# Kernel optimization log

Measured on AMD Instinct MI355X. Metric: run time of the kernel, lower is better.

## Reference

```python
import jax, jax.numpy as jnp
import numpy as np

NUM_BUCKETS = 320
MAX_DISTANCE = 800


def _layer_norm(x, w, b, eps=1e-5):
    x32 = x.astype(jnp.float32)
    mu = x32.mean(-1, keepdims=True)
    var = x32.var(-1, keepdims=True)
    return ((x32 - mu) / jnp.sqrt(var + eps) * w + b).astype(x.dtype)


def _rel_pos_bucket(rel):
    half = NUM_BUCKETS // 2            # 160
    st = half // 2                     # 80 (small threshold)
    sign = (rel >= 0).astype(jnp.int32)
    ab = jnp.abs(rel)
    is_small = ab < st
    log_ratio = jnp.log(jnp.clip(ab.astype(jnp.float32), 1.0) / st) / np.float32(np.log(MAX_DISTANCE / st))
    log_pos = st + (log_ratio * (half - st)).astype(jnp.int32)  # trunc toward zero like .long()
    log_pos = jnp.minimum(log_pos, half - 1)
    bucket = jnp.where(is_small, ab, log_pos) + sign * half
    return jnp.clip(bucket, 0, NUM_BUCKETS - 1)


def setup_inputs() -> dict:
    key = jax.random.key(0)
    B, T, C, H, FF = 2, 2048, 768, 12, 3072
    D = C // H
    ks = jax.random.split(key, 16)
    s = 0.02
    return {
        "x": jax.random.normal(ks[0], (B, T, C), jnp.float32),
        "ln1_w": jnp.ones((C,), jnp.float32),
        "ln1_b": jnp.zeros((C,), jnp.float32),
        "wq": jax.random.normal(ks[1], (C, C), jnp.float32) * s,
        "bq": jnp.zeros((C,), jnp.float32),
        "wk": jax.random.normal(ks[2], (C, C), jnp.float32) * s,
        "bk": jnp.zeros((C,), jnp.float32),
        "wv": jax.random.normal(ks[3], (C, C), jnp.float32) * s,
        "bv": jnp.zeros((C,), jnp.float32),
        "wo": jax.random.normal(ks[4], (C, C), jnp.float32) * s,
        "bo": jnp.zeros((C,), jnp.float32),
        "ln2_w": jnp.ones((C,), jnp.float32),
        "ln2_b": jnp.zeros((C,), jnp.float32),
        "w1": jax.random.normal(ks[5], (FF, C), jnp.float32) * s,
        "b1": jnp.zeros((FF,), jnp.float32),
        "w2": jax.random.normal(ks[6], (C, FF), jnp.float32) * s,
        "b2": jnp.zeros((C,), jnp.float32),
        "rel_embed": jax.random.normal(ks[7], (NUM_BUCKETS, H), jnp.float32),
        "gate_ur_w": jax.random.normal(ks[8], (H, D), jnp.float32) * 0.01,
        "gate_i_w": jax.random.normal(ks[9], (H, D), jnp.float32) * 0.01,
        "rel_scale": jnp.ones((H,), jnp.float32),
    }


def reference(x, ln1_w, ln1_b, wq, bq, wk, bk, wv, bv, wo, bo,
              ln2_w, ln2_b, w1, b1, w2, b2, rel_embed, gate_ur_w, gate_i_w, rel_scale):
    B, T, C = x.shape
    H = rel_embed.shape[1]
    D = C // H

    residual = x
    h = _layer_norm(x, ln1_w, ln1_b)
    q = (h @ wq.T + bq).reshape(B, T, H, D).transpose(0, 2, 1, 3)  # [B,H,T,D]
    k = (h @ wk.T + bk).reshape(B, T, H, D).transpose(0, 2, 1, 3)
    v = (h @ wv.T + bv).reshape(B, T, H, D).transpose(0, 2, 1, 3)

    attn = jnp.einsum('bhqd,bhkd->bhqk', q, k) * (D ** -0.5)

    # gated relative position bias
    pos = jnp.arange(T)
    rel = pos[None, :] - pos[:, None]                 # [T,T]
    buckets = _rel_pos_bucket(rel)                    # [T,T]
    pe = rel_embed[buckets]                           # [T,T,H]
    pe = jnp.transpose(pe, (2, 0, 1))[None]           # [1,H,T,T]
    g_in = q.mean(axis=2).transpose(0, 2, 1).mean(axis=-1)   # [B,D]
    gate_r = jax.nn.sigmoid(g_in @ gate_ur_w.T)       # [B,H]
    gate_u = jax.nn.sigmoid(g_in @ gate_i_w.T)        # [B,H]
    gate = 1.0 + (gate_u * rel_scale[None, :] * gate_r)[:, :, None, None]
    bias = pe * gate                                  # [B,H,T,T]

    attn = jax.nn.softmax(attn + bias, axis=-1)
    out = jnp.einsum('bhqk,bhkd->bhqd', attn, v).transpose(0, 2, 1, 3).reshape(B, T, C)
    x = residual + out @ wo.T + bo

    residual = x
    h = _layer_norm(x, ln2_w, ln2_b)
    h = jax.nn.gelu(h @ w1.T + b1, approximate=False) @ w2.T + b2
    return residual + h
```

## Files before the change

### kernel.cpp

```cpp
#include <hip/hip_runtime.h>
#include <hip/hip_bf16.h>


#define Tn 2048
#define Cn 768
#define Hn 12
#define Dn 64
#define FFn 3072
#define Mn 4096
#define QKVS 2304
#define LQK 1536

typedef __attribute__((ext_vector_type(8))) short bfrag;
typedef __attribute__((ext_vector_type(8))) unsigned short us8;
typedef __attribute__((ext_vector_type(4))) float f32x4;

#define GLDS(gptr, lptr) __builtin_amdgcn_global_load_lds( \
    (const __attribute__((address_space(1))) void*)(gptr), \
    (__attribute__((address_space(3))) void*)(lptr), 16, 0, 0)

__device__ __forceinline__ unsigned short f2bu(float f){
  __hip_bfloat16 h = __float2bfloat16(f);
  return *(unsigned short*)&h;
}
__device__ __forceinline__ float bu2f(unsigned short u){
  union { unsigned int i; float f; } v; v.i = ((unsigned int)u) << 16; return v.f;
}
__device__ __forceinline__ us8 pack8(float4 a, float4 b){
  us8 c;
  c[0]=f2bu(a.x); c[1]=f2bu(a.y); c[2]=f2bu(a.z); c[3]=f2bu(a.w);
  c[4]=f2bu(b.x); c[5]=f2bu(b.y); c[6]=f2bu(b.z); c[7]=f2bu(b.w);
  return c;
}
__device__ __forceinline__ float fexp2(float x){ return __builtin_amdgcn_exp2f(x); }

__device__ __forceinline__ float block_reduce_sum(float v, float* sred){
  #pragma unroll
  for (int off = 32; off > 0; off >>= 1) v += __shfl_down(v, off, 64);
  __syncthreads();
  if ((threadIdx.x & 63) == 0) sred[threadIdx.x >> 6] = v;
  __syncthreads();
  return sred[0] + sred[1] + sred[2] + sred[3];
}

__global__ __launch_bounds__(256) void cast_all_kernel(
    const float* __restrict__ wq, const float* __restrict__ wk,
    const float* __restrict__ wv, const float* __restrict__ wo,
    const float* __restrict__ w1, const float* __restrict__ w2,
    const float* __restrict__ bq, const float* __restrict__ bk,
    const float* __restrict__ bv,
    unsigned short* __restrict__ Wqkv, unsigned short* __restrict__ Wob,
    unsigned short* __restrict__ W1b, unsigned short* __restrict__ W2b,
    float* __restrict__ bqkv)
{
  const int blk = blockIdx.x;
  if (blk >= 3456){
    const int i = (blk - 3456) * 256 + threadIdx.x;
    bqkv[i] = (i < Cn) ? bq[i] : (i < 2 * Cn) ? bk[i - Cn] : bv[i - 2 * Cn];
    return;
  }
  const float* src; unsigned short* dst; int i;
  if (blk < 288)      { src = wq; dst = Wqkv;               i = blk * 256 + threadIdx.x; }
  else if (blk < 576) { src = wk; dst = Wqkv + Cn * Cn;     i = (blk - 288) * 256 + threadIdx.x; }
  else if (blk < 864) { src = wv; dst = Wqkv + 2 * Cn * Cn; i = (blk - 576) * 256 + threadIdx.x; }
  else if (blk < 1152){ src = wo; dst = Wob;                i = (blk - 864) * 256 + threadIdx.x; }
  else if (blk < 2304){ src = w1; dst = W1b;                i = (blk - 1152) * 256 + threadIdx.x; }
  else                { src = w2; dst = W2b;                i = (blk - 2304) * 256 + threadIdx.x; }
  const float4 a = ((const float4*)src)[i * 2];
  const float4 b = ((const float4*)src)[i * 2 + 1];
  *(us8*)&dst[i * 8] = pack8(a, b);
}

__global__ __launch_bounds__(256) void ln_kernel(const float* __restrict__ xin,
    const float* __restrict__ w, const float* __restrict__ bsh,
    unsigned short* __restrict__ out)
{
  __shared__ float xs[Cn];
  __shared__ float sred[4];
  const size_t base = (size_t)blockIdx.x * Cn;
  float s = 0.f;
  for (int c = threadIdx.x; c < Cn; c += 256){
    float v = xin[base + c];
    xs[c] = v; s += v;
  }
  const float mean = block_reduce_sum(s, sred) * (1.f / Cn);
  float s2 = 0.f;
  for (int c = threadIdx.x; c < Cn; c += 256){
    float d = xs[c] - mean; s2 += d * d;
  }
  const float var = block_reduce_sum(s2, sred) * (1.f / Cn);
  const float rstd = rsqrtf(var + 1e-5f);
  for (int c = threadIdx.x; c < Cn; c += 256)
    out[base + c] = f2bu((xs[c] - mean) * rstd * w[c] + bsh[c]);
}

template<int EPI, bool TRANSV>
__global__ __launch_bounds__(256) void gemm_mfma_kernel(
    const unsigned short* __restrict__ A, const unsigned short* __restrict__ Bw,
    const float* __restrict__ bias, unsigned short* __restrict__ vt,
    void* __restrict__ Cout, int M, int N, int K, int ldo)
{
  __shared__ __align__(16) unsigned short As[128 * 32];
  __shared__ __align__(16) unsigned short Bs[128 * 32];
  const int tid = threadIdx.x;
  const int lane = tid & 63, w = tid >> 6;
  const int nl = lane & 15, quad = lane >> 4;
  const int wm = w >> 1, wn = w & 1;
  const int bm = blockIdx.y * 128, bn = blockIdx.x * 128;
  const int l4 = lane >> 2, lk = (lane & 3) * 8;

  f32x4 acc[4][4];
  #pragma unroll
  for (int i = 0; i < 4; i++)
    #pragma unroll
    for (int j = 0; j < 4; j++) acc[i][j] = (f32x4){0.f, 0.f, 0.f, 0.f};

  const int c0 = w, c1 = w + 4;
  const unsigned short* A0 = A + (size_t)(bm + c0 * 16 + l4) * K + lk;
  const unsigned short* A1 = A + (size_t)(bm + c1 * 16 + l4) * K + lk;
  const unsigned short* B0 = Bw + (size_t)(bn + c0 * 16 + l4) * K + lk;
  const unsigned short* B1 = Bw + (size_t)(bn + c1 * 16 + l4) * K + lk;

  for (int k0 = 0; k0 < K; k0 += 32){
    __syncthreads();
    GLDS(A0 + k0, &As[c0 * 512]); GLDS(A1 + k0, &As[c1 * 512]);
    GLDS(B0 + k0, &Bs[c0 * 512]); GLDS(B1 + k0, &Bs[c1 * 512]);
    __syncthreads();
    bfrag Af[4], Bf[4];
    #pragma unroll
    for (int mt = 0; mt < 4; mt++)
      Af[mt] = *(const bfrag*)&As[(wm * 64 + mt * 16 + nl) * 32 + quad * 8];
    #pragma unroll
    for (int nt = 0; nt < 4; nt++)
      Bf[nt] = *(const bfrag*)&Bs[(wn * 64 + nt * 16 + nl) * 32 + quad * 8];
    #pragma unroll
    for (int mt = 0; mt < 4; mt++)
      #pragma unroll
      for (int nt = 0; nt < 4; nt++)
        acc[mt][nt] = __builtin_amdgcn_mfma_f32_16x16x32_bf16(Af[mt], Bf[nt], acc[mt][nt], 0, 0, 0);
  }

  if (TRANSV && bn >= 1536){
    #pragma unroll
    for (int nt = 0; nt < 4; nt++){
      const int col = bn + wn * 64 + nt * 16 + nl;
      const float bv_ = bias[col];
      const int vcol = col - 1536;
      #pragma unroll
      for (int mt = 0; mt < 4; mt++){
        const int row0 = bm + wm * 64 + mt * 16 + quad * 4;
        unsigned short pk[4];
        #pragma unroll
        for (int r = 0; r < 4; r++) pk[r] = f2bu(acc[mt][nt][r] + bv_);
        *(uint2*)&vt[(size_t)vcol * Mn + row0] = *(uint2*)pk;
      }
    }
    return;
  }
  #pragma unroll
  for (int nt = 0; nt < 4; nt++){
    const int col = bn + wn * 64 + nt * 16 + nl;
    const float bv_ = bias[col];
    #pragma unroll
    for (int mt = 0; mt < 4; mt++){
      const int row0 = bm + wm * 64 + mt * 16 + quad * 4;
      #pragma unroll
      for (int r = 0; r < 4; r++){
        const size_t idx = (size_t)(row0 + r) * ldo + col;
        const float v = acc[mt][nt][r] + bv_;
        if (EPI == 2){
          ((unsigned short*)Cout)[idx] = f2bu(0.5f * v * (1.f + erff(v * 0.70710678118f)));
        } else {
          ((unsigned short*)Cout)[idx] = f2bu(v);
        }
      }
    }
  }
}

__global__ __launch_bounds__(256) void gemm_t64_kernel(
    const unsigned short* __restrict__ A, const unsigned short* __restrict__ Bw,
    const float* __restrict__ bias, const float* __restrict__ res,
    float* __restrict__ Cout, int M, int N, int K)
{
  __shared__ __align__(16) unsigned short As[64 * 32];
  __shared__ __align__(16) unsigned short Bs[64 * 32];
  const int tid = threadIdx.x;
  const int lane = tid & 63, w = tid >> 6;
  const int nl = lane & 15, quad = lane >> 4;
  const int bm = blockIdx.y * 64, bn = blockIdx.x * 64;
  const int l4 = lane >> 2, lk = (lane & 3) * 8;

  f32x4 acc[4];
  #pragma unroll
  for (int j = 0; j < 4; j++) acc[j] = (f32x4){0.f, 0.f, 0.f, 0.f};

  const unsigned short* A0 = A + (size_t)(bm + w * 16 + l4) * K + lk;
  const unsigned short* B0 = Bw + (size_t)(bn + w * 16 + l4) * K + lk;

  for (int k0 = 0; k0 < K; k0 += 32){
    __syncthreads();
    GLDS(A0 + k0, &As[w * 512]);
    GLDS(B0 + k0, &Bs[w * 512]);
    __syncthreads();
    const bfrag Af = *(const bfrag*)&As[(w * 16 + nl) * 32 + quad * 8];
    bfrag Bf[4];
    #pragma unroll
    for (int nt = 0; nt < 4; nt++)
      Bf[nt] = *(const bfrag*)&Bs[(nt * 16 + nl) * 32 + quad * 8];
    #pragma unroll
    for (int nt = 0; nt < 4; nt++)
      acc[nt] = __builtin_amdgcn_mfma_f32_16x16x32_bf16(Af, Bf[nt], acc[nt], 0, 0, 0);
  }

  const int row0 = bm + w * 16 + quad * 4;
  #pragma unroll
  for (int nt = 0; nt < 4; nt++){
    const int col = bn + nt * 16 + nl;
    const float bv_ = bias[col];
    #pragma unroll
    for (int r = 0; r < 4; r++){
      const size_t idx = (size_t)(row0 + r) * N + col;
      Cout[idx] = acc[nt][r] + bv_ + res[idx];
    }
  }
}

__global__ __launch_bounds__(256) void qmean_part_kernel(
    const unsigned short* __restrict__ QKVqk, float* __restrict__ qpart)
{
  __shared__ float ps[Cn];
  const int b = blockIdx.y, t0 = blockIdx.x * 128;
  const int tid = threadIdx.x;
  float a0 = 0.f, a1 = 0.f, a2 = 0.f;
  for (int r = 0; r < 128; r++){
    const size_t base = (size_t)(b * Tn + t0 + r) * LQK;
    a0 += bu2f(QKVqk[base + tid]);
    a1 += bu2f(QKVqk[base + tid + 256]);
    a2 += bu2f(QKVqk[base + tid + 512]);
  }
  ps[tid] = a0; ps[tid + 256] = a1; ps[tid + 512] = a2;
  __syncthreads();
  if (tid < Dn){
    float s = 0.f;
    #pragma unroll
    for (int hh = 0; hh < Hn; hh++) s += ps[hh * Dn + tid];
    qpart[(b * 16 + blockIdx.x) * Dn + tid] = s;
  }
}

__global__ __launch_bounds__(64) void gate_kernel(const float* __restrict__ qpart,
    const float* __restrict__ gur, const float* __restrict__ gi,
    const float* __restrict__ rsc, float* __restrict__ gate)
{
  const int b = blockIdx.x / Hn, h = blockIdx.x % Hn;
  const int d = threadIdx.x;
  float s = 0.f;
  #pragma unroll
  for (int blk = 0; blk < 16; blk++) s += qpart[(b * 16 + blk) * Dn + d];
  const float g = s * (1.f / (Hn * Tn));
  float vr = g * gur[h * Dn + d];
  float vu = g * gi[h * Dn + d];
  #pragma unroll
  for (int off = 32; off > 0; off >>= 1){
    vr += __shfl_down(vr, off, 64);
    vu += __shfl_down(vu, off, 64);
  }
  if (d == 0){
    const float gr = 1.f / (1.f + __expf(-vr));
    const float gu = 1.f / (1.f + __expf(-vu));
    gate[blockIdx.x] = 1.f + gu * rsc[h] * gr;
  }
}

__global__ void bias_kernel(const float* __restrict__ rel_embed,
                            float* __restrict__ bias_rel)
{
  const int idx = blockIdx.x * 256 + threadIdx.x;
  if (idx >= 4095) return;
  const int rel = idx - 2047;
  const int ab = rel < 0 ? -rel : rel;
  int bucket;
  if (ab < 80){
    bucket = ab;
  } else {
    const float lr = logf((float)ab * (1.0f / 80.0f)) * (1.0f / 2.3025851f);
    int lp = 80 + (int)(lr * 80.0f);
    bucket = lp < 159 ? lp : 159;
  }
  if (rel >= 0) bucket += 160;
  #pragma unroll
  for (int h = 0; h < Hn; h++)
    bias_rel[h * 4095 + idx] = rel_embed[bucket * Hn + h] * 1.44269504089f;
}

__global__ __launch_bounds__(256) void attn_mfma_kernel(
    const unsigned short* __restrict__ QKVqk, const unsigned short* __restrict__ VT,
    const float* __restrict__ bias_rel, const float* __restrict__ gate,
    unsigned short* __restrict__ O)
{
  __shared__ __align__(16) char smem[9216 * 4 + 1024];
  unsigned short* Qs = (unsigned short*)smem;
  float* bias_blk    = (float*)smem;
  unsigned short* Ks = (unsigned short*)(smem + 9216);
  unsigned short* Vt = (unsigned short*)(smem + 18432);
  unsigned short* Ptq = (unsigned short*)(smem + 27648);
  float* lsh         = (float*)(smem + 36864);

  const int qbase = blockIdx.x * 64;
  const int h = blockIdx.y, b = blockIdx.z;
  const int tid = threadIdx.x;
  const float g = gate[b * Hn + h];
  const float* brow = bias_rel + h * 4095 + 1984 - qbase;
  const unsigned short* Q = QKVqk;
  const unsigned short* K = QKVqk + Cn;

  {
    const int row = tid >> 2, cg = (tid & 3) * 16;
    const us8* qp = (const us8*)(Q + (size_t)(b * Tn + qbase + row) * LQK + h * Dn + cg);
    *(us8*)&Qs[row * 72 + cg]     = qp[0];
    *(us8*)&Qs[row * 72 + cg + 8] = qp[1];
  }
  __syncthreads();

  const int lane = tid & 63, w = tid >> 6;
  const int nl = lane & 15, quad = lane >> 4;

  bfrag Qb[4][2];
  #pragma unroll
  for (int mt = 0; mt < 4; mt++){
    Qb[mt][0] = *(const bfrag*)&Qs[(mt * 16 + nl) * 72 + quad * 8];
    Qb[mt][1] = *(const bfrag*)&Qs[(mt * 16 + nl) * 72 + 32 + quad * 8];
  }
  __syncthreads();
  for (int j = tid; j < 2111; j += 256) bias_blk[j] = brow[j] * g;

  const int wq = w & 1, wd = w >> 1;
  f32x4 Oa[2][2];
  #pragma unroll
  for (int a = 0; a < 2; a++)
    #pragma unroll
    for (int d0 = 0; d0 < 2; d0++) Oa[a][d0] = (f32x4){0.f, 0.f, 0.f, 0.f};
  float l_part[4] = {0.f, 0.f, 0.f, 0.f};

  const int skey = tid >> 2, sdg = (tid & 3) * 16;
  const int vd = tid >> 3, vk8 = (tid & 7) * 8;
  const unsigned short* vtg = VT + (size_t)(h * Dn) * Mn + (size_t)b * Tn;

  for (int kt = 0; kt < 32; kt++){
    const int kbase = kt * 64;
    __syncthreads();
    {
      const us8* kp = (const us8*)(K + (size_t)(b * Tn + kbase + skey) * LQK + h * Dn + sdg);
      *(us8*)&Ks[skey * 72 + sdg]     = kp[0];
      *(us8*)&Ks[skey * 72 + sdg + 8] = kp[1];
    }
    {
      const us8 v0 = *(const us8*)&vtg[(size_t)vd * Mn + kbase + vk8];
      const us8 v1 = *(const us8*)&vtg[(size_t)(32 + vd) * Mn + kbase + vk8];
      *(us8*)&Vt[vd * 72 + vk8]        = v0;
      *(us8*)&Vt[(32 + vd) * 72 + vk8] = v1;
    }
    __syncthreads();

    const bfrag Ka0 = *(const bfrag*)&Ks[(w * 16 + nl) * 72 + quad * 8];
    const bfrag Ka1 = *(const bfrag*)&Ks[(w * 16 + nl) * 72 + 32 + quad * 8];
    const int bofs = kbase + w * 16 + quad * 4 + 63 - nl;
    #pragma unroll
    for (int mt = 0; mt < 4; mt++){
      f32x4 z = (f32x4){0.f, 0.f, 0.f, 0.f};
      z = __builtin_amdgcn_mfma_f32_16x16x32_bf16(Ka0, Qb[mt][0], z, 0, 0, 0);
      z = __builtin_amdgcn_mfma_f32_16x16x32_bf16(Ka1, Qb[mt][1], z, 0, 0, 0);
      unsigned short pk[4];
      #pragma unroll
      for (int r = 0; r < 4; r++){
        const float p = fexp2(z[r] * 0.18033688f + bias_blk[bofs - mt * 16 + r]);
        l_part[mt] += p;
        pk[r] = f2bu(p);
      }
      *(uint2*)&Ptq[(mt * 16 + nl) * 72 + w * 16 + quad * 4] = *(uint2*)pk;
    }
    __syncthreads();

    bfrag Vf[2][2], Pf[2][2];
    #pragma unroll
    for (int d0 = 0; d0 < 2; d0++){
      const int dt = wd * 2 + d0;
      Vf[d0][0] = *(const bfrag*)&Vt[(dt * 16 + nl) * 72 + quad * 8];
      Vf[d0][1] = *(const bfrag*)&Vt[(dt * 16 + nl) * 72 + 32 + quad * 8];
    }
    #pragma unroll
    for (int a = 0; a < 2; a++){
      const int qt = wq * 2 + a;
      Pf[a][0] = *(const bfrag*)&Ptq[(qt * 16 + nl) * 72 + quad * 8];
      Pf[a][1] = *(const bfrag*)&Ptq[(qt * 16 + nl) * 72 + 32 + quad * 8];
    }
    #pragma unroll
    for (int a = 0; a < 2; a++)
      #pragma unroll
      for (int d0 = 0; d0 < 2; d0++){
        Oa[a][d0] = __builtin_amdgcn_mfma_f32_16x16x32_bf16(Vf[d0][0], Pf[a][0], Oa[a][d0], 0, 0, 0);
        Oa[a][d0] = __builtin_amdgcn_mfma_f32_16x16x32_bf16(Vf[d0][1], Pf[a][1], Oa[a][d0], 0, 0, 0);
      }
  }

  #pragma unroll
  for (int mt = 0; mt < 4; mt++){
    float l = l_part[mt];
    l += __shfl_xor(l, 16, 64);
    l += __shfl_xor(l, 32, 64);
    if (quad == 0) lsh[w * 64 + mt * 16 + nl] = l;
  }
  __syncthreads();
  #pragma unroll
  for (int a = 0; a < 2; a++){
    const int q = (wq * 2 + a) * 16 + nl;
    const float linv = 1.f / (lsh[q] + lsh[64 + q] + lsh[128 + q] + lsh[192 + q]);
    unsigned short* orow = O + (size_t)(b * Tn + qbase + q) * Cn + h * Dn;
    #pragma unroll
    for (int d0 = 0; d0 < 2; d0++){
      unsigned short pk[4];
      #pragma unroll
      for (int r = 0; r < 4; r++) pk[r] = f2bu(Oa[a][d0][r] * linv);
      *(uint2*)&orow[(wd * 2 + d0) * 16 + quad * 4] = *(uint2*)pk;
    }
  }
}

extern "C" void kernel_launch(void* const* d_in, const int* in_sizes, int n_in,
                              void* d_out, int out_size, void* d_ws, size_t ws_size,
                              hipStream_t stream)
{
  const float* x     = (const float*)d_in[0];
  const float* ln1_w = (const float*)d_in[1];
  const float* ln1_b = (const float*)d_in[2];
  const float* wq    = (const float*)d_in[3];
  const float* bq    = (const float*)d_in[4];
  const float* wk    = (const float*)d_in[5];
  const float* bk    = (const float*)d_in[6];
  const float* wv    = (const float*)d_in[7];
  const float* bv    = (const float*)d_in[8];
  const float* wo    = (const float*)d_in[9];
  const float* bo    = (const float*)d_in[10];
  const float* ln2_w = (const float*)d_in[11];
  const float* ln2_b = (const float*)d_in[12];
  const float* w1    = (const float*)d_in[13];
  const float* b1    = (const float*)d_in[14];
  const float* w2    = (const float*)d_in[15];
  const float* b2    = (const float*)d_in[16];
  const float* rel_embed = (const float*)d_in[17];
  const float* gur   = (const float*)d_in[18];
  const float* gi    = (const float*)d_in[19];
  const float* rsc   = (const float*)d_in[20];

  char* ws = (char*)d_ws;
  unsigned short* QKVqk = (unsigned short*)(ws);
  unsigned short* VT    = (unsigned short*)(ws + 12582912);
  unsigned short* Ob    = (unsigned short*)(ws + 18874368);
  float*          X2    = (float*)(ws + 25165824);
  unsigned short* Hb    = (unsigned short*)(ws + 37748736);
  unsigned short* Wqkv  = (unsigned short*)(ws + 44040192);
  unsigned short* Wob   = (unsigned short*)(ws + 47579136);
  unsigned short* W1b   = (unsigned short*)(ws + 48758784);
  unsigned short* W2b   = (unsigned short*)(ws + 53477376);
  float*          bqkv  = (float*)(ws + 58195968);
  float*          bias_rel = (float*)(ws + 58205184);
  float*          qpart = (float*)(ws + 58401744);
  float*          gate  = (float*)(ws + 58409936);
  unsigned short* Fb    = (unsigned short*)(ws);

  cast_all_kernel<<<3465, 256, 0, stream>>>(wq, wk, wv, wo, w1, w2, bq, bk, bv,
                                            Wqkv, Wob, W1b, W2b, bqkv);
  ln_kernel<<<Mn, 256, 0, stream>>>(x, ln1_w, ln1_b, Hb);
  gemm_mfma_kernel<0, true><<<dim3(QKVS / 128, Mn / 128), 256, 0, stream>>>(
      Hb, Wqkv, bqkv, VT, QKVqk, Mn, QKVS, Cn, LQK);
  qmean_part_kernel<<<dim3(16, 2), 256, 0, stream>>>(QKVqk, qpart);
  gate_kernel<<<2 * Hn, 64, 0, stream>>>(qpart, gur, gi, rsc, gate);
  bias_kernel<<<16, 256, 0, stream>>>(rel_embed, bias_rel);
  attn_mfma_kernel<<<dim3(Tn / 64, Hn, 2), 256, 0, stream>>>(QKVqk, VT, bias_rel, gate, Ob);
  gemm_t64_kernel<<<dim3(Cn / 64, Mn / 64), 256, 0, stream>>>(
      Ob, Wob, bo, x, X2, Mn, Cn, Cn);
  ln_kernel<<<Mn, 256, 0, stream>>>(X2, ln2_w, ln2_b, Hb);
  gemm_mfma_kernel<2, false><<<dim3(FFn / 128, Mn / 128), 256, 0, stream>>>(
      Hb, W1b, b1, nullptr, Fb, Mn, FFn, Cn, FFn);
  gemm_t64_kernel<<<dim3(Cn / 64, Mn / 64), 256, 0, stream>>>(
      Fb, W2b, b2, X2, (float*)d_out, Mn, Cn, FFn);
}
```

Baseline: 356.3 us.

## Precompute fragment-ordered rel-pos bias table and swizzle GEMM block order

Replaces the per-head 1D bias vector, which each attention block staged into LDS, with a larger table precomputed inside the cast kernel. The table is laid out per (head, q-block diagonal, k-offset, lane) so each lane reads a float4 directly from global memory. This removes the LDS staging, its sync and the scalar LDS reads, and drops the separate bias kernel launch. The gate multiply becomes an fma, and the GEMM kernels now remap a 1D grid so consecutive blocks share B tiles for better L2 reuse. The cost is a ~5MB bias table read from global/L2 inside the attention inner loop.

```diff
diff --git a/kernel.cpp b/kernel.cpp
--- a/kernel.cpp
+++ b/kernel.cpp
@@ -43,20 +43,52 @@
   return sred[0] + sred[1] + sred[2] + sred[3];
 }
 
+__device__ __forceinline__ int rel_bucket(int rel){
+  const int ab = rel < 0 ? -rel : rel;
+  int bucket;
+  if (ab < 80){
+    bucket = ab;
+  } else {
+    const float lr = logf((float)ab * (1.0f / 80.0f)) * (1.0f / 2.3025851f);
+    int lp = 80 + (int)(lr * 80.0f);
+    bucket = lp < 159 ? lp : 159;
+  }
+  if (rel >= 0) bucket += 160;
+  return bucket;
+}
+
 __global__ __launch_bounds__(256) void cast_all_kernel(
     const float* __restrict__ wq, const float* __restrict__ wk,
     const float* __restrict__ wv, const float* __restrict__ wo,
     const float* __restrict__ w1, const float* __restrict__ w2,
     const float* __restrict__ bq, const float* __restrict__ bk,
-    const float* __restrict__ bv,
+    const float* __restrict__ bv, const float* __restrict__ rel_embed,
     unsigned short* __restrict__ Wqkv, unsigned short* __restrict__ Wob,
     unsigned short* __restrict__ W1b, unsigned short* __restrict__ W2b,
-    float* __restrict__ bqkv)
+    float* __restrict__ biasT, float* __restrict__ bqkv)
 {
   const int blk = blockIdx.x;
+  if (blk >= 3787){
+    const int i = (blk - 3787) * 256 + threadIdx.x;
+    bqkv[i] = (i < Cn) ? bq[i] : (i < 2 * Cn) ? bk[i - Cn] : bv[i - 2 * Cn];
+    return;
+  }
   if (blk >= 3456){
-    const int i = (blk - 3456) * 256 + threadIdx.x;
-    bqkv[i] = (i < Cn) ? bq[i] : (i < 2 * Cn) ? bk[i - Cn] : bv[i - 2 * Cn];
+    const int f4 = (blk - 3456) * 256 + threadIdx.x;
+    if (f4 >= 84672) return;
+    int t = f4;
+    const int nl = t & 15; t >>= 4;
+    const int quad = t & 3; t >>= 2;
+    const int dmi = t % 7; t /= 7;
+    const int di = t % 63; t /= 63;
+    const int h = t;
+    const int rbase = 64 * (di - 31) + 16 * (dmi - 3) + quad * 4 - nl;
+    float4 o;
+    o.x = rel_embed[rel_bucket(rbase + 0) * Hn + h] * 1.44269504089f;
+    o.y = rel_embed[rel_bucket(rbase + 1) * Hn + h] * 1.44269504089f;
+    o.z = rel_embed[rel_bucket(rbase + 2) * Hn + h] * 1.44269504089f;
+    o.w = rel_embed[rel_bucket(rbase + 3) * Hn + h] * 1.44269504089f;
+    ((float4*)biasT)[f4] = o;
     return;
   }
   const float* src; unsigned short* dst; int i;
@@ -106,7 +138,9 @@
   const int lane = tid & 63, w = tid >> 6;
   const int nl = lane & 15, quad = lane >> 4;
   const int wm = w >> 1, wn = w & 1;
-  const int bm = blockIdx.y * 128, bn = blockIdx.x * 128;
+  const int id = blockIdx.x;
+  const int bm = ((id & 7) * 4 + ((id >> 3) & 3)) * 128;
+  const int bn = (id >> 5) * 128;
   const int l4 = lane >> 2, lk = (lane & 3) * 8;
 
   f32x4 acc[4][4];
@@ -188,7 +222,9 @@
   const int tid = threadIdx.x;
   const int lane = tid & 63, w = tid >> 6;
   const int nl = lane & 15, quad = lane >> 4;
-  const int bm = blockIdx.y * 64, bn = blockIdx.x * 64;
+  const int id = blockIdx.x;
+  const int bm = ((id & 7) * 8 + ((id >> 3) & 7)) * 64;
+  const int bn = (id >> 6) * 64;
   const int l4 = lane >> 2, lk = (lane & 3) * 8;
 
   f32x4 acc[4];
@@ -273,45 +309,21 @@
   }
 }
 
-__global__ void bias_kernel(const float* __restrict__ rel_embed,
-                            float* __restrict__ bias_rel)
-{
-  const int idx = blockIdx.x * 256 + threadIdx.x;
-  if (idx >= 4095) return;
-  const int rel = idx - 2047;
-  const int ab = rel < 0 ? -rel : rel;
-  int bucket;
-  if (ab < 80){
-    bucket = ab;
-  } else {
-    const float lr = logf((float)ab * (1.0f / 80.0f)) * (1.0f / 2.3025851f);
-    int lp = 80 + (int)(lr * 80.0f);
-    bucket = lp < 159 ? lp : 159;
-  }
-  if (rel >= 0) bucket += 160;
-  #pragma unroll
-  for (int h = 0; h < Hn; h++)
-    bias_rel[h * 4095 + idx] = rel_embed[bucket * Hn + h] * 1.44269504089f;
-}
-
 __global__ __launch_bounds__(256) void attn_mfma_kernel(
     const unsigned short* __restrict__ QKVqk, const unsigned short* __restrict__ VT,
-    const float* __restrict__ bias_rel, const float* __restrict__ gate,
+    const float* __restrict__ biasT, const float* __restrict__ gate,
     unsigned short* __restrict__ O)
 {
-  __shared__ __align__(16) char smem[9216 * 4 + 1024];
-  unsigned short* Qs = (unsigned short*)smem;
-  float* bias_blk    = (float*)smem;
-  unsigned short* Ks = (unsigned short*)(smem + 9216);
-  unsigned short* Vt = (unsigned short*)(smem + 18432);
-  unsigned short* Ptq = (unsigned short*)(smem + 27648);
-  float* lsh         = (float*)(smem + 36864);
-
-  const int qbase = blockIdx.x * 64;
+  __shared__ __align__(16) unsigned short Qs[64 * 72];
+  __shared__ __align__(16) unsigned short Ks[64 * 72];
+  __shared__ __align__(16) unsigned short Vt[64 * 72];
+  __shared__ __align__(16) unsigned short Ptq[64 * 72];
+  __shared__ float lsh[4 * 64];
+
+  const int qblk = blockIdx.x, qbase = qblk * 64;
   const int h = blockIdx.y, b = blockIdx.z;
   const int tid = threadIdx.x;
   const float g = gate[b * Hn + h];
-  const float* brow = bias_rel + h * 4095 + 1984 - qbase;
   const unsigned short* Q = QKVqk;
   const unsigned short* K = QKVqk + Cn;
 
@@ -332,8 +344,9 @@
     Qb[mt][0] = *(const bfrag*)&Qs[(mt * 16 + nl) * 72 + quad * 8];
     Qb[mt][1] = *(const bfrag*)&Qs[(mt * 16 + nl) * 72 + 32 + quad * 8];
   }
-  __syncthreads();
-  for (int j = tid; j < 2111; j += 256) bias_blk[j] = brow[j] * g;
+
+  const float* bT0 = biasT
+      + (((size_t)(h * 63 + 31 - qblk) * 7) + 3 + w) * 256 + quad * 64 + nl * 4;
 
   const int wq = w & 1, wd = w >> 1;
   f32x4 Oa[2][2];
@@ -365,19 +378,20 @@
 
     const bfrag Ka0 = *(const bfrag*)&Ks[(w * 16 + nl) * 72 + quad * 8];
     const bfrag Ka1 = *(const bfrag*)&Ks[(w * 16 + nl) * 72 + 32 + quad * 8];
-    const int bofs = kbase + w * 16 + quad * 4 + 63 - nl;
+    const float* bTk = bT0 + (size_t)kt * 1792;
     #pragma unroll
     for (int mt = 0; mt < 4; mt++){
       f32x4 z = (f32x4){0.f, 0.f, 0.f, 0.f};
       z = __builtin_amdgcn_mfma_f32_16x16x32_bf16(Ka0, Qb[mt][0], z, 0, 0, 0);
       z = __builtin_amdgcn_mfma_f32_16x16x32_bf16(Ka1, Qb[mt][1], z, 0, 0, 0);
+      const float4 bv = *(const float4*)(bTk - mt * 256);
       unsigned short pk[4];
-      #pragma unroll
-      for (int r = 0; r < 4; r++){
-        const float p = fexp2(z[r] * 0.18033688f + bias_blk[bofs - mt * 16 + r]);
-        l_part[mt] += p;
-        pk[r] = f2bu(p);
-      }
+      const float p0 = fexp2(fmaf(bv.x, g, z[0] * 0.18033688f));
+      const float p1 = fexp2(fmaf(bv.y, g, z[1] * 0.18033688f));
+      const float p2 = fexp2(fmaf(bv.z, g, z[2] * 0.18033688f));
+      const float p3 = fexp2(fmaf(bv.w, g, z[3] * 0.18033688f));
+      l_part[mt] += p0 + p1 + p2 + p3;
+      pk[0] = f2bu(p0); pk[1] = f2bu(p1); pk[2] = f2bu(p2); pk[3] = f2bu(p3);
       *(uint2*)&Ptq[(mt * 16 + nl) * 72 + w * 16 + quad * 4] = *(uint2*)pk;
     }
     __syncthreads();
@@ -464,25 +478,25 @@
   unsigned short* W1b   = (unsigned short*)(ws + 48758784);
   unsigned short* W2b   = (unsigned short*)(ws + 53477376);
   float*          bqkv  = (float*)(ws + 58195968);
-  float*          bias_rel = (float*)(ws + 58205184);
-  float*          qpart = (float*)(ws + 58401744);
-  float*          gate  = (float*)(ws + 58409936);
+  float*          biasT = (float*)(ws + 58205184);
+  float*          qpart = (float*)(ws + 63624192);
+  float*          gate  = (float*)(ws + 63632384);
   unsigned short* Fb    = (unsigned short*)(ws);
 
-  cast_all_kernel<<<3465, 256, 0, stream>>>(wq, wk, wv, wo, w1, w2, bq, bk, bv,
-                                            Wqkv, Wob, W1b, W2b, bqkv);
+  cast_all_kernel<<<3796, 256, 0, stream>>>(wq, wk, wv, wo, w1, w2, bq, bk, bv,
+                                            rel_embed, Wqkv, Wob, W1b, W2b,
+                                            biasT, bqkv);
   ln_kernel<<<Mn, 256, 0, stream>>>(x, ln1_w, ln1_b, Hb);
-  gemm_mfma_kernel<0, true><<<dim3(QKVS / 128, Mn / 128), 256, 0, stream>>>(
+  gemm_mfma_kernel<0, true><<<(QKVS / 128) * (Mn / 128), 256, 0, stream>>>(
       Hb, Wqkv, bqkv, VT, QKVqk, Mn, QKVS, Cn, LQK);
   qmean_part_kernel<<<dim3(16, 2), 256, 0, stream>>>(QKVqk, qpart);
   gate_kernel<<<2 * Hn, 64, 0, stream>>>(qpart, gur, gi, rsc, gate);
-  bias_kernel<<<16, 256, 0, stream>>>(rel_embed, bias_rel);
-  attn_mfma_kernel<<<dim3(Tn / 64, Hn, 2), 256, 0, stream>>>(QKVqk, VT, bias_rel, gate, Ob);
-  gemm_t64_kernel<<<dim3(Cn / 64, Mn / 64), 256, 0, stream>>>(
+  attn_mfma_kernel<<<dim3(Tn / 64, Hn, 2), 256, 0, stream>>>(QKVqk, VT, biasT, gate, Ob);
+  gemm_t64_kernel<<<(Cn / 64) * (Mn / 64), 256, 0, stream>>>(
       Ob, Wob, bo, x, X2, Mn, Cn, Cn);
   ln_kernel<<<Mn, 256, 0, stream>>>(X2, ln2_w, ln2_b, Hb);
-  gemm_mfma_kernel<2, false><<<dim3(FFn / 128, Mn / 128), 256, 0, stream>>>(
+  gemm_mfma_kernel<2, false><<<(FFn / 128) * (Mn / 128), 256, 0, stream>>>(
       Hb, W1b, b1, nullptr, Fb, Mn, FFn, Cn, FFn);
-  gemm_t64_kernel<<<dim3(Cn / 64, Mn / 64), 256, 0, stream>>>(
+  gemm_t64_kernel<<<(Cn / 64) * (Mn / 64), 256, 0, stream>>>(
       Fb, W2b, b2, X2, (float*)d_out, Mn, Cn, FFn);
 }
```

New measurement: 370.9 us. 1.04x slower.
